# Performance work log

Hardware: AMD Instinct MI355X
Metric: run time of the kernel (lower is better)

## Reference

```python
import jax, jax.numpy as jnp
import numpy as np

N_SAMPLES = 10
DROPOUT_P = 0.1
EPS = 1e-12
B, F, C = 32768, 512, 1000


def setup_inputs() -> dict:
    key = jax.random.key(0)
    k1, k2, k3, k4 = jax.random.split(key, 4)
    return {
        "features": jax.random.normal(k1, (B, F), dtype=jnp.float32),
        "logits": jax.random.normal(k2, (B, C), dtype=jnp.float32),
        "W": jax.random.normal(k3, (F, C), dtype=jnp.float32) * 0.05,
        "b": jax.random.normal(k4, (C,), dtype=jnp.float32) * 0.05,
    }


def reference(features, logits, W, b):
    # `logits` is part of the provider interface but unused by this provider.
    del logits
    keep_p = 1.0 - DROPOUT_P
    mask_key = jax.random.key(42)
    # (n_samples, batch, feat) Bernoulli keep masks; inverted-dropout scaling.
    masks = jax.random.bernoulli(mask_key, keep_p, (N_SAMPLES,) + features.shape)
    dropped = jnp.where(masks, features[None] / keep_p, 0.0)  # (S, B, F)
    lgts = jnp.einsum("sbf,fc->sbc", dropped, W) + b          # (S, B, C)
    probs = jax.nn.softmax(lgts, axis=-1)                      # (S, B, C)
    mean = jnp.mean(probs, axis=0)                             # (B, C)
    # torch .var(dim=0) uses unbiased (n-1) normalization.
    var = jnp.sum((probs - mean[None]) ** 2, axis=0) / (N_SAMPLES - 1)
    total_var = jnp.sum(var, axis=-1, keepdims=True)           # (B, 1)
    # Scaler not fitted -> _normalize is identity.
    return jnp.log(total_var + EPS)
```

## Files before the change

### kernel.cpp

```cpp
#include <hip/hip_runtime.h>
#include <hip/hip_bf16.h>
#include <stdint.h>
#include <math.h>

typedef __attribute__((ext_vector_type(8))) short short8;
typedef __attribute__((ext_vector_type(4))) float f32x4;

namespace {
constexpr int kB = 32768;
constexpr int kF = 512;
constexpr int kC = 1000;
constexpr int kCpad = 1024;
constexpr int kS = 10;
constexpr int G = 8;
constexpr int M = G * kS;
constexpr int MT = M / 16;
constexpr int NTW = 8;
constexpr int WAVES = 8;
constexpr int SK = 64;
constexpr int SLICES = kF / SK;
constexpr uint32_t SLICE_BYTES = M * SK * 2;
constexpr uint32_t kKeepThr = 3865470464u;
}

__device__ __forceinline__ uint32_t rotl32(uint32_t x, uint32_t r) {
#if __has_builtin(__builtin_rotateleft32)
  return __builtin_rotateleft32(x, r);
#else
  return (x << r) | (x >> (32u - r));
#endif
}

__device__ __forceinline__ uint32_t threefry2x32_xor(uint32_t c0, uint32_t c1) {
  const uint32_t ks0 = 0u;
  const uint32_t ks1 = 42u;
  const uint32_t ks2 = 0x1BD11BDAu ^ ks0 ^ ks1;
  uint32_t x0 = c0 + ks0;
  uint32_t x1 = c1 + ks1;
#define TF_ROUND(r) { x0 += x1; x1 = rotl32(x1, r); x1 ^= x0; }
  TF_ROUND(13u) TF_ROUND(15u) TF_ROUND(26u) TF_ROUND(6u)
  x0 += ks1; x1 += ks2 + 1u;
  TF_ROUND(17u) TF_ROUND(29u) TF_ROUND(16u) TF_ROUND(24u)
  x0 += ks2; x1 += ks0 + 2u;
  TF_ROUND(13u) TF_ROUND(15u) TF_ROUND(26u) TF_ROUND(6u)
  x0 += ks0; x1 += ks1 + 3u;
  TF_ROUND(17u) TF_ROUND(29u) TF_ROUND(16u) TF_ROUND(24u)
  x0 += ks1; x1 += ks2 + 4u;
  TF_ROUND(13u) TF_ROUND(15u) TF_ROUND(26u) TF_ROUND(6u)
  x0 += ks2; x1 += ks0 + 5u;
#undef TF_ROUND
  return x0 ^ x1;
}

__device__ __forceinline__ uint32_t f2bf(float x) {
  uint32_t u = __float_as_uint(x);
  return (u + 0x7fffu + ((u >> 16) & 1u)) >> 16;
}

__device__ __forceinline__ uint32_t pack_bf16x2(float lo, float hi) {
  uint32_t r;
  asm("v_cvt_pk_bf16_f32 %0, %1, %2" : "=v"(r) : "v"(lo), "v"(hi));
  return r;
}


__global__ __launch_bounds__(256) void prep_wt(const float* __restrict__ W,
                                               ushort* __restrict__ Wt) {
  __shared__ float tile[64][65];
  const int kt = blockIdx.x * 64;
  const int ct = blockIdx.y * 64;
  const int tid = threadIdx.x;
#pragma unroll
  for (int i = 0; i < 16; ++i) {
    const int lin = i * 256 + tid;
    const int rk = lin >> 6, cc = lin & 63;
    const int gc = ct + cc;
    tile[rk][cc] = (gc < kC) ? W[(size_t)(kt + rk) * kC + gc] : 0.0f;
  }
  __syncthreads();
#pragma unroll
  for (int i = 0; i < 8; ++i) {
    const int lin = i * 256 + tid;
    const int cc = lin >> 5, kp = lin & 31;
    const int gc = ct + cc;
    const uint32_t lo = f2bf(tile[kp * 2][cc]);
    const uint32_t hi = f2bf(tile[kp * 2 + 1][cc]);
    ((uint32_t*)Wt)[(size_t)gc * (kF / 2) + (kt >> 1) + kp] = lo | (hi << 16);
  }
}

__global__ __launch_bounds__(256) void prep_bias(const float* __restrict__ b,
                                                 float* __restrict__ biasp) {
  const int i = blockIdx.x * 256 + threadIdx.x;
  if (i < kCpad) biasp[i] = (i < kC) ? b[i] : -INFINITY;
}


__global__ __launch_bounds__(512, 2) void mc_mfma_kernel(
    const float* __restrict__ features, const ushort* __restrict__ Wt,
    const float* __restrict__ biasp, float* __restrict__ out) {
  __shared__ __align__(16) ushort Abuf[2][M * SK];
  __shared__ float wred[M][9];
  __shared__ float rowinv[M];
  __shared__ float part[G][9];

  const int tid = threadIdx.x;
  const int b0 = blockIdx.x * G;
  const int wv = tid >> 6;
  const int lane = tid & 63;
  const int cp = lane & 15;
  const int gr = lane >> 4;
  const int cbase = wv * 128;

  const int fp = tid & 31;
  const int mbase = tid >> 5;
  const int gg = mbase & 7;
  const int s0 = mbase >> 3;
  char* const Ab0 = (char*)&Abuf[0][0];

  const uint32_t idx_row =
      (uint32_t)s0 * (uint32_t)(kB * kF) + (uint32_t)(b0 + gg) * kF +
      (uint32_t)(fp * 2);
  const uint32_t swz_off =
      ((uint32_t)(mbase * 128 + fp * 4)) ^ ((uint32_t)gg << 4);
  const float2* const fbase =
      (const float2*)features + ((uint32_t)(b0 + gg) * (kF / 2) + fp);

  auto gen_dword = [&](uint32_t idxb, uint32_t byteb, int i, float f0,
                       float f1) {
    const uint32_t c1 = idxb + ((uint32_t)i << 25);
    const uint32_t bits0 = threefry2x32_xor(0u, c1);
    const uint32_t bits1 = threefry2x32_xor(0u, c1 + 1u);
    const float a0 = (bits0 < kKeepThr) ? f0 : 0.0f;
    const float a1 = (bits1 < kKeepThr) ? f1 : 0.0f;
    *(uint32_t*)(Ab0 + byteb + (uint32_t)(i * 2048)) = pack_bf16x2(a0, a1);
  };

  f32x4 acc[MT][NTW];
#pragma unroll
  for (int mt = 0; mt < MT; ++mt)
#pragma unroll
    for (int nt = 0; nt < NTW; ++nt)
#pragma unroll
      for (int r = 0; r < 4; ++r) acc[mt][nt][r] = 0.0f;

  const uint32_t wbase = (uint32_t)(cbase + cp) * kF + (uint32_t)(gr * 8);
  const uint32_t aswz = (uint32_t)((cp & 7) << 4);
  const uint32_t arow = (uint32_t)(cp * 128);

  {
    const float2 fv = fbase[0];
    const float f0 = fv.x * (1.0f / 0.9f);
    const float f1 = fv.y * (1.0f / 0.9f);
#pragma unroll
    for (int i = 0; i < 5; ++i) gen_dword(idx_row, swz_off, i, f0, f1);
  }
  __syncthreads();

#define MFMA_CHUNK(n0, n1, A, BF)                                       \
  __builtin_amdgcn_s_setprio(1);                                        \
  _Pragma("unroll")                                                     \
  for (int nt = (n0); nt < (n1); ++nt)                                  \
    _Pragma("unroll")                                                   \
    for (int mt = 0; mt < MT; ++mt)                                     \
      acc[mt][nt] = __builtin_amdgcn_mfma_f32_16x16x32_bf16(            \
          (A)[mt], (BF)[nt], acc[mt][nt], 0, 0, 0);                     \
  __builtin_amdgcn_s_setprio(0);

#pragma unroll 1
  for (int sl = 0; sl < SLICES; ++sl) {
    const uint32_t cur = (uint32_t)(sl & 1) * SLICE_BYTES;
    const uint32_t wsl = wbase + (uint32_t)(sl * SK);
    const char* Ar = (const char*)Ab0 + cur;
    const bool has_next = (sl + 1 < SLICES);

    const float2 fv = fbase[((sl + 1) & 7) * 32];
    const float f0 = fv.x * (1.0f / 0.9f);
    const float f1 = fv.y * (1.0f / 0.9f);
    const uint32_t idxb = idx_row + (uint32_t)((sl + 1) * SK);
    const uint32_t byteb = (cur ^ SLICE_BYTES) + swz_off;

    short8 bf[NTW];
#pragma unroll
    for (int nt = 0; nt < NTW; ++nt)
      bf[nt] = *(const short8*)(Wt + wsl + (uint32_t)nt * 8192u);
    short8 a[MT];
#pragma unroll
    for (int mt = 0; mt < MT; ++mt)
      a[mt] = *(const short8*)(Ar + (uint32_t)(mt * 2048) + arow +
                               (((uint32_t)(gr * 16)) ^ aswz));

    MFMA_CHUNK(0, 2, a, bf)
    if (has_next) gen_dword(idxb, byteb, 0, f0, f1);
    MFMA_CHUNK(2, 4, a, bf)
    if (has_next) gen_dword(idxb, byteb, 1, f0, f1);
    MFMA_CHUNK(4, 6, a, bf)
    if (has_next) gen_dword(idxb, byteb, 2, f0, f1);
    MFMA_CHUNK(6, 8, a, bf)

#pragma unroll
    for (int nt = 0; nt < NTW; ++nt)
      bf[nt] = *(const short8*)(Wt + wsl + 32u + (uint32_t)nt * 8192u);
#pragma unroll
    for (int mt = 0; mt < MT; ++mt)
      a[mt] = *(const short8*)(Ar + (uint32_t)(mt * 2048) + arow +
                               (((uint32_t)(64 + gr * 16)) ^ aswz));

    MFMA_CHUNK(0, 3, a, bf)
    if (has_next) gen_dword(idxb, byteb, 3, f0, f1);
    MFMA_CHUNK(3, 6, a, bf)
    if (has_next) gen_dword(idxb, byteb, 4, f0, f1);
    MFMA_CHUNK(6, 8, a, bf)

    __syncthreads();
  }
#undef MFMA_CHUNK

  const float* bp = biasp + cbase + cp;
  float bias_lane[NTW];
#pragma unroll
  for (int nt = 0; nt < NTW; ++nt) bias_lane[nt] = bp[nt * 16];

  float red[MT][4];
#pragma unroll
  for (int mt = 0; mt < MT; ++mt)
#pragma unroll
    for (int r = 0; r < 4; ++r) {
      float z = 0.0f;
#pragma unroll
      for (int nt = 0; nt < NTW; ++nt) {
        const float e = __expf(acc[mt][nt][r] + bias_lane[nt]);
        acc[mt][nt][r] = e;
        z += e;
      }
      red[mt][r] = z;
    }
#pragma unroll
  for (int off = 1; off <= 8; off <<= 1)
#pragma unroll
    for (int mt = 0; mt < MT; ++mt)
#pragma unroll
      for (int r = 0; r < 4; ++r) red[mt][r] += __shfl_xor(red[mt][r], off);
  if (cp == 0) {
#pragma unroll
    for (int mt = 0; mt < MT; ++mt)
#pragma unroll
      for (int r = 0; r < 4; ++r) wred[mt * 16 + gr * 4 + r][wv] = red[mt][r];
  }
  __syncthreads();
  if (tid < M) {
    float z = 0.0f;
#pragma unroll
    for (int w = 0; w < WAVES; ++w) z += wred[tid][w];
    rowinv[tid] = 1.0f / z;
  }
  __syncthreads();

#pragma unroll
  for (int mt = 0; mt < MT; ++mt)
#pragma unroll
    for (int r = 0; r < 4; ++r) red[mt][r] = rowinv[mt * 16 + gr * 4 + r];

  float vp[4] = {0.0f, 0.0f, 0.0f, 0.0f};
#pragma unroll
  for (int nt = 0; nt < NTW; ++nt)
#pragma unroll
    for (int r = 0; r < 4; ++r) {
      float sp = 0.0f, sp2 = 0.0f;
#pragma unroll
      for (int mt = 0; mt < MT; ++mt) {
        const float p = acc[mt][nt][r] * red[mt][r];
        sp += p;
        sp2 += p * p;
      }
      sp += __shfl_xor(sp, 32);
      sp2 += __shfl_xor(sp2, 32);
      vp[r] += sp2 - sp * sp * 0.1f;
    }
#pragma unroll
  for (int off = 1; off <= 8; off <<= 1)
#pragma unroll
    for (int r = 0; r < 4; ++r) vp[r] += __shfl_xor(vp[r], off);
  if (cp == 0 && gr < 2) {
#pragma unroll
    for (int r = 0; r < 4; ++r) part[gr * 4 + r][wv] = vp[r];
  }
  __syncthreads();
  if (tid < G) {
    float t = 0.0f;
#pragma unroll
    for (int w = 0; w < WAVES; ++w) t += part[tid][w];
    t = fmaxf(t, 0.0f);
    out[b0 + tid] = logf(t * (1.0f / 9.0f) + 1e-12f);
  }
}


template <bool IS_MAX>
__device__ __forceinline__ float block_reduce(float v, float* red) {
#pragma unroll
  for (int off = 32; off >= 1; off >>= 1) {
    const float o = __shfl_xor(v, off);
    v = IS_MAX ? fmaxf(v, o) : (v + o);
  }
  const int wid = threadIdx.x >> 6;
  if ((threadIdx.x & 63) == 0) red[wid] = v;
  __syncthreads();
  float r = red[0];
#pragma unroll
  for (int w = 1; w < 4; ++w) r = IS_MAX ? fmaxf(r, red[w]) : (r + red[w]);
  __syncthreads();
  return r;
}

__global__ __launch_bounds__(256) void mc_dropout_var_kernel(
    const float* __restrict__ features, const float* __restrict__ W,
    const float* __restrict__ bias, float* __restrict__ out) {
  const int b = blockIdx.x;
  const int tid = threadIdx.x;
  __shared__ float mf[kS][kF];
  __shared__ float red[4];
  const uint32_t row_base = (uint32_t)b * (uint32_t)kF;
  for (int k = 0; k < (kS * kF) / 256; ++k) {
    const int lin = k * 256 + tid;
    const int s = lin >> 9;
    const int f = lin & (kF - 1);
    const uint32_t idx =
        (uint32_t)s * (uint32_t)(kB * kF) + row_base + (uint32_t)f;
    const uint32_t bits = threefry2x32_xor(0u, idx);
    const float u = __uint_as_float((bits >> 9) | 0x3f800000u) - 1.0f;
    const float fv = features[row_base + f];
    mf[s][f] = (u < 0.9f) ? (fv / 0.9f) : 0.0f;
  }
  __syncthreads();
  const bool active = (tid < kC / 4);
  const int c0 = tid * 4;
  float acc[kS][4];
#pragma unroll
  for (int s = 0; s < kS; ++s)
#pragma unroll
    for (int j = 0; j < 4; ++j) acc[s][j] = 0.0f;
  if (active) {
    const float* wp = W + c0;
    for (int f = 0; f < kF; f += 4) {
      float wv[4][4];
      *reinterpret_cast<float4*>(wv[0]) =
          *reinterpret_cast<const float4*>(wp + (size_t)(f + 0) * kC);
      *reinterpret_cast<float4*>(wv[1]) =
          *reinterpret_cast<const float4*>(wp + (size_t)(f + 1) * kC);
      *reinterpret_cast<float4*>(wv[2]) =
          *reinterpret_cast<const float4*>(wp + (size_t)(f + 2) * kC);
      *reinterpret_cast<float4*>(wv[3]) =
          *reinterpret_cast<const float4*>(wp + (size_t)(f + 3) * kC);
#pragma unroll
      for (int s = 0; s < kS; ++s) {
        float mm[4];
        *reinterpret_cast<float4*>(mm) =
            *reinterpret_cast<const float4*>(&mf[s][f]);
#pragma unroll
        for (int j = 0; j < 4; ++j) {
#pragma unroll
          for (int q = 0; q < 4; ++q)
            acc[s][j] = fmaf(mm[q], wv[q][j], acc[s][j]);
        }
      }
    }
  }
  float bias_r[4] = {0.f, 0.f, 0.f, 0.f};
  if (active) {
    const float4 bb = *reinterpret_cast<const float4*>(bias + c0);
    bias_r[0] = bb.x; bias_r[1] = bb.y; bias_r[2] = bb.z; bias_r[3] = bb.w;
  }
  float sum_p[4] = {0.f, 0.f, 0.f, 0.f};
  float sum_p2[4] = {0.f, 0.f, 0.f, 0.f};
#pragma unroll 1
  for (int s = 0; s < kS; ++s) {
    float l[4] = {0.f, 0.f, 0.f, 0.f};
    float lmax = -INFINITY;
    if (active) {
#pragma unroll
      for (int j = 0; j < 4; ++j) {
        l[j] = acc[s][j] + bias_r[j];
        lmax = fmaxf(lmax, l[j]);
      }
    }
    const float bmax = block_reduce<true>(lmax, red);
    float psum = 0.f;
    float p[4] = {0.f, 0.f, 0.f, 0.f};
    if (active) {
#pragma unroll
      for (int j = 0; j < 4; ++j) {
        p[j] = expf(l[j] - bmax);
        psum += p[j];
      }
    }
    const float bsum = block_reduce<false>(psum, red);
    const float inv = 1.0f / bsum;
    if (active) {
#pragma unroll
      for (int j = 0; j < 4; ++j) {
        const float pr = p[j] * inv;
        sum_p[j] += pr;
        sum_p2[j] += pr * pr;
      }
    }
  }
  float partv = 0.f;
  if (active) {
#pragma unroll
    for (int j = 0; j < 4; ++j)
      partv += (sum_p2[j] - sum_p[j] * sum_p[j] * 0.1f) * (1.0f / 9.0f);
  }
  const float total = block_reduce<false>(partv, red);
  if (tid == 0) out[b] = logf(total + 1e-12f);
}


extern "C" void kernel_launch(void* const* d_in, const int* in_sizes, int n_in,
                              void* d_out, int out_size, void* d_ws, size_t ws_size,
                              hipStream_t stream) {
  const float* features = (const float*)d_in[0];
  const float* W = (const float*)d_in[2];
  const float* bias = (const float*)d_in[3];
  float* out = (float*)d_out;

  const size_t wt_bytes = (size_t)kCpad * kF * sizeof(ushort);
  const size_t need = wt_bytes + (size_t)kCpad * sizeof(float);

  if (ws_size >= need) {
    ushort* Wt = (ushort*)d_ws;
    float* biasp = (float*)((char*)d_ws + wt_bytes);
    hipLaunchKernelGGL(prep_wt, dim3(kF / 64, kCpad / 64), dim3(256), 0, stream,
                       W, Wt);
    hipLaunchKernelGGL(prep_bias, dim3((kCpad + 255) / 256), dim3(256), 0,
                       stream, bias, biasp);
    hipLaunchKernelGGL(mc_mfma_kernel, dim3(kB / G), dim3(512), 0, stream,
                       features, Wt, biasp, out);
  } else {
    hipLaunchKernelGGL(mc_dropout_var_kernel, dim3(kB), dim3(256), 0, stream,
                       features, W, bias, out);
  }
}
```

Before: 798.8 us.

## Use 16 waves per block with narrower column tiles and deeper K slices

Doubles the block to 16 waves, each covering 64 classes (4 N-tiles) instead of 128, and doubles the K slice to 128 so there are half as many barriers. The dropout mask generation is redistributed so each wave produces one row of the A tile. The MFMA inner loop is restructured to load A fragments per M-tile and interleave mask generation between K sub-steps under explicit sched_barriers. This trades fewer accumulator registers per wave and more waves for latency hiding against larger LDS usage, dropping the 2-blocks-per-SM launch bound hint, and redundant A loads across more waves.

```diff
diff --git a/kernel.cpp b/kernel.cpp
--- a/kernel.cpp
+++ b/kernel.cpp
@@ -15,9 +15,10 @@
 constexpr int G = 8;
 constexpr int M = G * kS;
 constexpr int MT = M / 16;
-constexpr int NTW = 8;
-constexpr int WAVES = 8;
-constexpr int SK = 64;
+constexpr int NTW = 4;
+constexpr int WAVES = 16;
+constexpr int NTHREADS = WAVES * 64;
+constexpr int SK = 128;
 constexpr int SLICES = kF / SK;
 constexpr uint32_t SLICE_BYTES = M * SK * 2;
 constexpr uint32_t kKeepThr = 3865470464u;
@@ -96,13 +97,13 @@
 }
 
 
-__global__ __launch_bounds__(512, 2) void mc_mfma_kernel(
+__global__ __launch_bounds__(NTHREADS) void mc_mfma_kernel(
     const float* __restrict__ features, const ushort* __restrict__ Wt,
     const float* __restrict__ biasp, float* __restrict__ out) {
   __shared__ __align__(16) ushort Abuf[2][M * SK];
-  __shared__ float wred[M][9];
+  __shared__ float wred[M][WAVES + 1];
   __shared__ float rowinv[M];
-  __shared__ float part[G][9];
+  __shared__ float part[G][WAVES + 1];
 
   const int tid = threadIdx.x;
   const int b0 = blockIdx.x * G;
@@ -110,21 +111,19 @@
   const int lane = tid & 63;
   const int cp = lane & 15;
   const int gr = lane >> 4;
-  const int cbase = wv * 128;
-
-  const int fp = tid & 31;
-  const int mbase = tid >> 5;
-  const int gg = mbase & 7;
-  const int s0 = mbase >> 3;
+  const int cbase = wv * 64;
   char* const Ab0 = (char*)&Abuf[0][0];
 
+  const int dcol = tid & 63;
+  const int rbase = wv;
+  const int gg = rbase & 7;
+  const int s0 = rbase >> 3;
   const uint32_t idx_row =
-      (uint32_t)s0 * (uint32_t)(kB * kF) + (uint32_t)(b0 + gg) * kF +
-      (uint32_t)(fp * 2);
+      ((uint32_t)s0 << 24) + (uint32_t)(b0 + gg) * kF + (uint32_t)(dcol * 2);
   const uint32_t swz_off =
-      ((uint32_t)(mbase * 128 + fp * 4)) ^ ((uint32_t)gg << 4);
+      ((uint32_t)(rbase * 256 + dcol * 4)) ^ ((uint32_t)gg << 4);
   const float2* const fbase =
-      (const float2*)features + ((uint32_t)(b0 + gg) * (kF / 2) + fp);
+      (const float2*)features + ((uint32_t)(b0 + gg) * (kF / 2) + dcol);
 
   auto gen_dword = [&](uint32_t idxb, uint32_t byteb, int i, float f0,
                        float f1) {
@@ -133,7 +132,7 @@
     const uint32_t bits1 = threefry2x32_xor(0u, c1 + 1u);
     const float a0 = (bits0 < kKeepThr) ? f0 : 0.0f;
     const float a1 = (bits1 < kKeepThr) ? f1 : 0.0f;
-    *(uint32_t*)(Ab0 + byteb + (uint32_t)(i * 2048)) = pack_bf16x2(a0, a1);
+    *(uint32_t*)(Ab0 + byteb + (uint32_t)(i * 4096)) = pack_bf16x2(a0, a1);
   };
 
   f32x4 acc[MT][NTW];
@@ -146,7 +145,7 @@
 
   const uint32_t wbase = (uint32_t)(cbase + cp) * kF + (uint32_t)(gr * 8);
   const uint32_t aswz = (uint32_t)((cp & 7) << 4);
-  const uint32_t arow = (uint32_t)(cp * 128);
+  const uint32_t arow = (uint32_t)(cp * 256);
 
   {
     const float2 fv = fbase[0];
@@ -157,15 +156,32 @@
   }
   __syncthreads();
 
-#define MFMA_CHUNK(n0, n1, A, BF)                                       \
-  __builtin_amdgcn_s_setprio(1);                                        \
-  _Pragma("unroll")                                                     \
-  for (int nt = (n0); nt < (n1); ++nt)                                  \
-    _Pragma("unroll")                                                   \
-    for (int mt = 0; mt < MT; ++mt)                                     \
-      acc[mt][nt] = __builtin_amdgcn_mfma_f32_16x16x32_bf16(            \
-          (A)[mt], (BF)[nt], acc[mt][nt], 0, 0, 0);                     \
-  __builtin_amdgcn_s_setprio(0);
+#define KK_STEP(kk, NGEN, IBASE)                                          \
+  {                                                                       \
+    short8 bf[NTW];                                                       \
+    _Pragma("unroll")                                                     \
+    for (int nt = 0; nt < NTW; ++nt)                                      \
+      bf[nt] = *(const short8*)(Wt + wsl + (uint32_t)((kk) * 32) +        \
+                                (uint32_t)nt * 8192u);                    \
+    if (has_next) {                                                       \
+      _Pragma("unroll")                                                   \
+      for (int i = 0; i < (NGEN); ++i)                                    \
+        gen_dword(idxb, byteb, (IBASE) + i, f0, f1);                      \
+    }                                                                     \
+    __builtin_amdgcn_sched_barrier(0);                                    \
+    __builtin_amdgcn_s_setprio(1);                                        \
+    _Pragma("unroll")                                                     \
+    for (int mt = 0; mt < MT; ++mt) {                                     \
+      const short8 a = *(const short8*)(                                  \
+          Ar + (uint32_t)(mt * 4096) + arow +                             \
+          (((uint32_t)((kk) * 64 + gr * 16)) ^ aswz));                    \
+      _Pragma("unroll")                                                   \
+      for (int nt = 0; nt < NTW; ++nt)                                    \
+        acc[mt][nt] = __builtin_amdgcn_mfma_f32_16x16x32_bf16(            \
+            a, bf[nt], acc[mt][nt], 0, 0, 0);                             \
+    }                                                                     \
+    __builtin_amdgcn_s_setprio(0);                                        \
+  }
 
 #pragma unroll 1
   for (int sl = 0; sl < SLICES; ++sl) {
@@ -174,47 +190,20 @@
     const char* Ar = (const char*)Ab0 + cur;
     const bool has_next = (sl + 1 < SLICES);
 
-    const float2 fv = fbase[((sl + 1) & 7) * 32];
+    const float2 fv = fbase[((sl + 1) & 3) * 64];
     const float f0 = fv.x * (1.0f / 0.9f);
     const float f1 = fv.y * (1.0f / 0.9f);
     const uint32_t idxb = idx_row + (uint32_t)((sl + 1) * SK);
     const uint32_t byteb = (cur ^ SLICE_BYTES) + swz_off;
 
-    short8 bf[NTW];
-#pragma unroll
-    for (int nt = 0; nt < NTW; ++nt)
-      bf[nt] = *(const short8*)(Wt + wsl + (uint32_t)nt * 8192u);
-    short8 a[MT];
-#pragma unroll
-    for (int mt = 0; mt < MT; ++mt)
-      a[mt] = *(const short8*)(Ar + (uint32_t)(mt * 2048) + arow +
-                               (((uint32_t)(gr * 16)) ^ aswz));
-
-    MFMA_CHUNK(0, 2, a, bf)
-    if (has_next) gen_dword(idxb, byteb, 0, f0, f1);
-    MFMA_CHUNK(2, 4, a, bf)
-    if (has_next) gen_dword(idxb, byteb, 1, f0, f1);
-    MFMA_CHUNK(4, 6, a, bf)
-    if (has_next) gen_dword(idxb, byteb, 2, f0, f1);
-    MFMA_CHUNK(6, 8, a, bf)
-
-#pragma unroll
-    for (int nt = 0; nt < NTW; ++nt)
-      bf[nt] = *(const short8*)(Wt + wsl + 32u + (uint32_t)nt * 8192u);
-#pragma unroll
-    for (int mt = 0; mt < MT; ++mt)
-      a[mt] = *(const short8*)(Ar + (uint32_t)(mt * 2048) + arow +
-                               (((uint32_t)(64 + gr * 16)) ^ aswz));
-
-    MFMA_CHUNK(0, 3, a, bf)
-    if (has_next) gen_dword(idxb, byteb, 3, f0, f1);
-    MFMA_CHUNK(3, 6, a, bf)
-    if (has_next) gen_dword(idxb, byteb, 4, f0, f1);
-    MFMA_CHUNK(6, 8, a, bf)
+    KK_STEP(0, 2, 0)
+    KK_STEP(1, 1, 2)
+    KK_STEP(2, 1, 3)
+    KK_STEP(3, 1, 4)
 
     __syncthreads();
   }
-#undef MFMA_CHUNK
+#undef KK_STEP
 
   const float* bp = biasp + cbase + cp;
   float bias_lane[NTW];
@@ -434,7 +423,7 @@
                        W, Wt);
     hipLaunchKernelGGL(prep_bias, dim3((kCpad + 255) / 256), dim3(256), 0,
                        stream, bias, biasp);
-    hipLaunchKernelGGL(mc_mfma_kernel, dim3(kB / G), dim3(512), 0, stream,
+    hipLaunchKernelGGL(mc_mfma_kernel, dim3(kB / G), dim3(NTHREADS), 0, stream,
                        features, Wt, biasp, out);
   } else {
     hipLaunchKernelGGL(mc_dropout_var_kernel, dim3(kB), dim3(256), 0, stream,
```

Result: slower. 984.9 us (+23.3%).

## Stagger PRNG mask generation and MFMA phases across wave groups

Applied to the files above, without the earlier changes.

Splits the waves into two groups with opposite schedules inside each K-slice. One group runs PRNG mask generation first and then its MFMAs, while the other does MFMAs first and PRNG afterwards. Scheduling barriers pin this order. The aim is to keep the matrix units busy while the other group is doing integer hash work, instead of interleaving both inside every wave. The cost is extra code and divergent per-wave schedules, and the result depends on waves sharing the same SIMD.

```diff
diff --git a/kernel.cpp b/kernel.cpp
--- a/kernel.cpp
+++ b/kernel.cpp
@@ -147,6 +147,7 @@
   const uint32_t wbase = (uint32_t)(cbase + cp) * kF + (uint32_t)(gr * 8);
   const uint32_t aswz = (uint32_t)((cp & 7) << 4);
   const uint32_t arow = (uint32_t)(cp * 128);
+  const bool grp0 = ((wv >> 2) & 1) == 0;
 
   {
     const float2 fv = fbase[0];
@@ -157,15 +158,37 @@
   }
   __syncthreads();
 
-#define MFMA_CHUNK(n0, n1, A, BF)                                       \
-  __builtin_amdgcn_s_setprio(1);                                        \
-  _Pragma("unroll")                                                     \
-  for (int nt = (n0); nt < (n1); ++nt)                                  \
-    _Pragma("unroll")                                                   \
-    for (int mt = 0; mt < MT; ++mt)                                     \
-      acc[mt][nt] = __builtin_amdgcn_mfma_f32_16x16x32_bf16(            \
-          (A)[mt], (BF)[nt], acc[mt][nt], 0, 0, 0);                     \
-  __builtin_amdgcn_s_setprio(0);
+#define SB __builtin_amdgcn_sched_barrier(0)
+#define B_LO(kofs)                                                        \
+  { _Pragma("unroll") for (int nt = 0; nt < 4; ++nt)                      \
+      bfA[nt] = *(const short8*)(Wt + wsl + (kofs) + (uint32_t)nt * 8192u); }
+#define B_HI(kofs)                                                        \
+  { _Pragma("unroll") for (int nt = 0; nt < 4; ++nt)                      \
+      bfB[nt] = *(const short8*)(Wt + wsl + (kofs) +                      \
+                                 (uint32_t)(nt + 4) * 8192u); }
+#define A_RD(kbyte)                                                       \
+  { _Pragma("unroll") for (int mt = 0; mt < MT; ++mt)                     \
+      a[mt] = *(const short8*)(Ar + (uint32_t)(mt * 2048) + arow +        \
+                               (((uint32_t)((kbyte) + gr * 16)) ^ aswz)); }
+#define MFMA_LO                                                           \
+  { __builtin_amdgcn_s_setprio(1);                                        \
+    _Pragma("unroll") for (int nt = 0; nt < 4; ++nt)                      \
+      _Pragma("unroll") for (int mt = 0; mt < MT; ++mt)                   \
+        acc[mt][nt] = __builtin_amdgcn_mfma_f32_16x16x32_bf16(            \
+            a[mt], bfA[nt], acc[mt][nt], 0, 0, 0);                        \
+    __builtin_amdgcn_s_setprio(0); }
+#define MFMA_HI                                                           \
+  { __builtin_amdgcn_s_setprio(1);                                        \
+    _Pragma("unroll") for (int nt = 4; nt < 8; ++nt)                      \
+      _Pragma("unroll") for (int mt = 0; mt < MT; ++mt)                   \
+        acc[mt][nt] = __builtin_amdgcn_mfma_f32_16x16x32_bf16(            \
+            a[mt], bfB[nt - 4], acc[mt][nt], 0, 0, 0);                    \
+    __builtin_amdgcn_s_setprio(0); }
+#define PRNG3 if (has_next) { gen_dword(idxb, byteb, 0, f0, f1);          \
+                              gen_dword(idxb, byteb, 1, f0, f1);          \
+                              gen_dword(idxb, byteb, 2, f0, f1); }
+#define PRNG2 if (has_next) { gen_dword(idxb, byteb, 3, f0, f1);          \
+                              gen_dword(idxb, byteb, 4, f0, f1); }
 
 #pragma unroll 1
   for (int sl = 0; sl < SLICES; ++sl) {
@@ -180,41 +203,52 @@
     const uint32_t idxb = idx_row + (uint32_t)((sl + 1) * SK);
     const uint32_t byteb = (cur ^ SLICE_BYTES) + swz_off;
 
-    short8 bf[NTW];
-#pragma unroll
-    for (int nt = 0; nt < NTW; ++nt)
-      bf[nt] = *(const short8*)(Wt + wsl + (uint32_t)nt * 8192u);
+    short8 bfA[4], bfB[4];
     short8 a[MT];
-#pragma unroll
-    for (int mt = 0; mt < MT; ++mt)
-      a[mt] = *(const short8*)(Ar + (uint32_t)(mt * 2048) + arow +
-                               (((uint32_t)(gr * 16)) ^ aswz));
-
-    MFMA_CHUNK(0, 2, a, bf)
-    if (has_next) gen_dword(idxb, byteb, 0, f0, f1);
-    MFMA_CHUNK(2, 4, a, bf)
-    if (has_next) gen_dword(idxb, byteb, 1, f0, f1);
-    MFMA_CHUNK(4, 6, a, bf)
-    if (has_next) gen_dword(idxb, byteb, 2, f0, f1);
-    MFMA_CHUNK(6, 8, a, bf)
-
-#pragma unroll
-    for (int nt = 0; nt < NTW; ++nt)
-      bf[nt] = *(const short8*)(Wt + wsl + 32u + (uint32_t)nt * 8192u);
-#pragma unroll
-    for (int mt = 0; mt < MT; ++mt)
-      a[mt] = *(const short8*)(Ar + (uint32_t)(mt * 2048) + arow +
-                               (((uint32_t)(64 + gr * 16)) ^ aswz));
-
-    MFMA_CHUNK(0, 3, a, bf)
-    if (has_next) gen_dword(idxb, byteb, 3, f0, f1);
-    MFMA_CHUNK(3, 6, a, bf)
-    if (has_next) gen_dword(idxb, byteb, 4, f0, f1);
-    MFMA_CHUNK(6, 8, a, bf)
-
+
+    if (grp0) {
+      B_LO(0u)
+      PRNG3
+      SB;
+      B_HI(0u)
+      A_RD(0)
+      MFMA_LO
+      MFMA_HI
+      SB;
+      B_LO(32u)
+      PRNG2
+      SB;
+      B_HI(32u)
+      A_RD(64)
+      MFMA_LO
+      MFMA_HI
+    } else {
+      B_LO(0u)
+      A_RD(0)
+      MFMA_LO
+      B_HI(0u)
+      MFMA_HI
+      SB;
+      PRNG3
+      SB;
+      B_LO(32u)
+      A_RD(64)
+      MFMA_LO
+      B_HI(32u)
+      MFMA_HI
+      SB;
+      PRNG2
+    }
     __syncthreads();
   }
-#undef MFMA_CHUNK
+#undef SB
+#undef B_LO
+#undef B_HI
+#undef A_RD
+#undef MFMA_LO
+#undef MFMA_HI
+#undef PRNG3
+#undef PRNG2
 
   const float* bp = biasp + cbase + cp;
   float bias_lane[NTW];
```

After: 726.5 us. -9.1%, faster.
